# Kernel tuning notes

Hardware: AMD Instinct MI355X
Metric: run time of the kernel (lower is better)

## Reference

```python
import jax, jax.numpy as jnp
import numpy as np

NUM_CLASSES = 4   # Level has 4 contiguous classes 0..3
VMAX = 64         # discretized vital-sign codes live in [0, VMAX)
HID = 64
OUT = 768
IN_VS = 28


def casual_weighted(vs, labels):
    """Vectorized equivalent of Encoder.CasualWeighted.

    For row i, col c: prob = (# rows j with labels[j]==labels[i] and
    vs[j,c]==vs[i,c]) / (# rows with labels==labels[i]).  Returns vs * prob.
    """
    N, F = vs.shape
    vs_int = vs.astype(jnp.int32)                       # values are integer codes
    lab = labels.astype(jnp.int32)
    keys = lab[:, None] * VMAX + vs_int                 # [N, F] joint (class, value) key
    cols = jnp.arange(F)[None, :]                       # [1, F]
    counts = jnp.zeros((NUM_CLASSES * VMAX, F), jnp.float32).at[keys, cols].add(1.0)
    class_size = jnp.zeros((NUM_CLASSES,), jnp.float32).at[lab].add(1.0)
    prob = counts[keys, cols] / class_size[lab][:, None]  # [N, F]
    return vs * prob


def feature_extractor(x, W_ih, W_hh, b_ih, b_hh, W_fc, b_fc):
    """nn.LSTM over a length-1 sequence (h0=c0=0) followed by Linear."""
    h0 = jnp.zeros((x.shape[0], HID), x.dtype)
    gates = x @ W_ih.T + h0 @ W_hh.T + b_ih + b_hh      # [N, 4H], torch gate order i,f,g,o
    i, f, g, o = jnp.split(gates, 4, axis=-1)
    c = jax.nn.sigmoid(i) * jnp.tanh(g)                 # f*c0 = 0
    h = jax.nn.sigmoid(o) * jnp.tanh(c)
    return h @ W_fc.T + b_fc                            # [N, OUT]


def setup_inputs() -> dict:
    key = jax.random.key(0)
    ks = jax.random.split(key, 10)
    N = 100000
    VS = jax.random.randint(ks[0], (N, IN_VS), 0, VMAX).astype(jnp.float32)
    CC = jax.random.normal(ks[1], (N, 1, OUT), dtype=jnp.float32)
    Level = jax.random.randint(ks[2], (N,), 0, NUM_CLASSES).astype(jnp.int64)
    Depart = jax.random.randint(ks[3], (N,), 0, 10).astype(jnp.int64)
    s = 0.05
    W_ih = jax.random.normal(ks[4], (4 * HID, IN_VS), dtype=jnp.float32) * s
    W_hh = jax.random.normal(ks[5], (4 * HID, HID), dtype=jnp.float32) * s
    b_ih = jax.random.normal(ks[6], (4 * HID,), dtype=jnp.float32) * s
    b_hh = jax.random.normal(ks[7], (4 * HID,), dtype=jnp.float32) * s
    W_fc = jax.random.normal(ks[8], (OUT, HID), dtype=jnp.float32) * s
    b_fc = jax.random.normal(ks[9], (OUT,), dtype=jnp.float32) * s
    return {"VS": VS, "CC": CC, "Level": Level, "Depart": Depart,
            "W_ih": W_ih, "W_hh": W_hh, "b_ih": b_ih, "b_hh": b_hh,
            "W_fc": W_fc, "b_fc": b_fc}


def reference(VS, CC, Level, Depart, W_ih, W_hh, b_ih, b_hh, W_fc, b_fc):
    cc_feat = jnp.squeeze(CC)                           # [N, 768]
    vs_cw = casual_weighted(VS, Level)                  # [N, 28]
    vs_feat = feature_extractor(vs_cw, W_ih, W_hh, b_ih, b_hh, W_fc, b_fc)
    return (cc_feat, vs_feat, Level, Depart)
```

## Files before the change

kernel.cpp:

```cpp
#include <hip/hip_runtime.h>
#include <hip/hip_bf16.h>

#define N_ROWS 100000
#define F_VS 28
#define HIDN 64
#define OUT_F 768
#define NCLS 4
#define VMAXC 64

typedef __attribute__((ext_vector_type(8))) short short8;
typedef __attribute__((ext_vector_type(4))) float floatx4;


__device__ __forceinline__ float frcp(float x) { return __builtin_amdgcn_rcpf(x); }
__device__ __forceinline__ float sigm(float x) { return frcp(1.f + __expf(-x)); }
__device__ __forceinline__ float tanh_f(float x) { return 1.f - 2.f * frcp(__expf(2.f * x) + 1.f); }

__global__ __launch_bounds__(256) void k_hist(const float* __restrict__ VS,
                                              const int* __restrict__ Level,
                                              const float* __restrict__ Wfc,
                                              int* __restrict__ counts,
                                              int* __restrict__ cls,
                                              __hip_bfloat16* __restrict__ wfc16) {
    __shared__ int lc[NCLS * VMAXC * F_VS];
    __shared__ int lcls[NCLS];
    int tid = threadIdx.x;
    for (int i = tid; i < NCLS * VMAXC * F_VS; i += 256) lc[i] = 0;
    if (tid < NCLS) lcls[tid] = 0;

    int gtid = blockIdx.x * 256 + tid;
    int gsz = gridDim.x * 256;
    for (int i = gtid; i < OUT_F * HIDN; i += gsz)
        wfc16[i] = __float2bfloat16(Wfc[i]);
    __syncthreads();

    for (int i = gtid; i < N_ROWS; i += gsz) {
        int lab = Level[i];
        atomicAdd(&lcls[lab], 1);
        const float4* row = (const float4*)(VS + (size_t)i * F_VS);
#pragma unroll
        for (int q = 0; q < 7; q++) {
            float4 v4 = row[q];
            int c = q * 4;
            atomicAdd(&lc[((lab << 6) + (int)v4.x) * F_VS + c + 0], 1);
            atomicAdd(&lc[((lab << 6) + (int)v4.y) * F_VS + c + 1], 1);
            atomicAdd(&lc[((lab << 6) + (int)v4.z) * F_VS + c + 2], 1);
            atomicAdd(&lc[((lab << 6) + (int)v4.w) * F_VS + c + 3], 1);
        }
    }
    __syncthreads();
    for (int i = tid; i < NCLS * VMAXC * F_VS; i += 256) {
        int v = lc[i];
        if (v) atomicAdd(&counts[i], v);
    }
    if (tid < NCLS) {
        int v = lcls[tid];
        if (v) atomicAdd(&cls[tid], v);
    }
}

__global__ __launch_bounds__(256) void k_lstm(const float* __restrict__ VS,
                                              const int* __restrict__ Level,
                                              const int* __restrict__ Depart,
                                              const float* __restrict__ Wih,
                                              const float* __restrict__ bih,
                                              const float* __restrict__ bhh,
                                              const int* __restrict__ counts,
                                              const int* __restrict__ cls,
                                              __hip_bfloat16* __restrict__ h16,
                                              float* __restrict__ outL,
                                              float* __restrict__ outD) {
    int tid = threadIdx.x;
    int gtid = blockIdx.x * 256 + tid;

    if (gtid < N_ROWS) {
        outL[gtid] = (float)Level[gtid];
        outD[gtid] = (float)Depart[gtid];
    }

    int lane = tid & 63;
    int wib = tid >> 6;
    int w = gtid >> 6;
    int nw = (gridDim.x * 256) >> 6;

    float w0[F_VS], w2[F_VS], w3[F_VS];
#pragma unroll
    for (int j = 0; j < F_VS; j++) {
        w0[j] = Wih[(0 * HIDN + lane) * F_VS + j];
        w2[j] = Wih[(2 * HIDN + lane) * F_VS + j];
        w3[j] = Wih[(3 * HIDN + lane) * F_VS + j];
    }
    float b0 = bih[0 * HIDN + lane] + bhh[0 * HIDN + lane];
    float b2 = bih[2 * HIDN + lane] + bhh[2 * HIDN + lane];
    float b3 = bih[3 * HIDN + lane] + bhh[3 * HIDN + lane];

    __shared__ float xsh[4][64];

    for (int r = w; r < N_ROWS; r += nw) {
        int lab = Level[r];
        float inv = frcp((float)cls[lab]);
        float xv = 0.f;
        if (lane < F_VS) {
            float v = VS[(size_t)r * F_VS + lane];
            int vi = (int)v;
            int cnt = counts[(((lab << 6) | vi)) * F_VS + lane];
            xv = v * ((float)cnt * inv);
        }
        xsh[wib][lane] = xv;
        __asm__ volatile("" ::: "memory");

        float a0 = b0, a2 = b2, a3 = b3;
#pragma unroll
        for (int q = 0; q < 7; q++) {
            floatx4 xq = *(const floatx4*)(&xsh[wib][q * 4]);
            a0 = fmaf(xq[0], w0[4 * q + 0], a0);
            a0 = fmaf(xq[1], w0[4 * q + 1], a0);
            a0 = fmaf(xq[2], w0[4 * q + 2], a0);
            a0 = fmaf(xq[3], w0[4 * q + 3], a0);
            a2 = fmaf(xq[0], w2[4 * q + 0], a2);
            a2 = fmaf(xq[1], w2[4 * q + 1], a2);
            a2 = fmaf(xq[2], w2[4 * q + 2], a2);
            a2 = fmaf(xq[3], w2[4 * q + 3], a2);
            a3 = fmaf(xq[0], w3[4 * q + 0], a3);
            a3 = fmaf(xq[1], w3[4 * q + 1], a3);
            a3 = fmaf(xq[2], w3[4 * q + 2], a3);
            a3 = fmaf(xq[3], w3[4 * q + 3], a3);
        }
        __asm__ volatile("" ::: "memory");

        float c = sigm(a0) * tanh_f(a2);
        float h = sigm(a3) * tanh_f(c);
        h16[(size_t)r * HIDN + lane] = __float2bfloat16(h);
    }
}

__global__ __launch_bounds__(256) void k_gemm(const __hip_bfloat16* __restrict__ h16,
                                              const __hip_bfloat16* __restrict__ wfc16,
                                              const float* __restrict__ bfc,
                                              float* __restrict__ outV) {
    int tid = threadIdx.x;
    int lane = tid & 63;
    int w = (blockIdx.x * 256 + tid) >> 6;
    int nw = (gridDim.x * 256) >> 6;
    int quad = lane >> 4;
    int l16 = lane & 15;
    const int nm = N_ROWS / 16;

    for (int mt = w; mt < nm; mt += nw) {
        int row0 = mt * 16;
        const short* hA = (const short*)(h16 + (size_t)(row0 + l16) * HIDN + quad * 8);
        short8 a0 = *(const short8*)(hA);
        short8 a1 = *(const short8*)(hA + 32);
        for (int nt = 0; nt < OUT_F / 16; nt++) {
            const short* pB = (const short*)(wfc16 + (size_t)(nt * 16 + l16) * HIDN + quad * 8);
            short8 bf0 = *(const short8*)(pB);
            short8 bf1 = *(const short8*)(pB + 32);
            floatx4 acc = {0.f, 0.f, 0.f, 0.f};
            acc = __builtin_amdgcn_mfma_f32_16x16x32_bf16(a0, bf0, acc, 0, 0, 0);
            acc = __builtin_amdgcn_mfma_f32_16x16x32_bf16(a1, bf1, acc, 0, 0, 0);
            float bias = bfc[nt * 16 + l16];
#pragma unroll
            for (int rr = 0; rr < 4; rr++) {
                outV[(size_t)(row0 + quad * 4 + rr) * OUT_F + nt * 16 + l16] = acc[rr] + bias;
            }
        }
    }
}

__global__ __launch_bounds__(256) void k_copy(const float4* __restrict__ src,
                                              float4* __restrict__ dst, int n4) {
    int i = blockIdx.x * blockDim.x + threadIdx.x;
    int s = gridDim.x * blockDim.x;
    for (; i < n4; i += s) dst[i] = src[i];
}

extern "C" void kernel_launch(void* const* d_in, const int* in_sizes, int n_in,
                              void* d_out, int out_size, void* d_ws, size_t ws_size,
                              hipStream_t stream) {
    const float* VS = (const float*)d_in[0];
    const float* CC = (const float*)d_in[1];
    const int* Level = (const int*)d_in[2];
    const int* Depart = (const int*)d_in[3];
    const float* Wih = (const float*)d_in[4];
    const float* bih = (const float*)d_in[6];
    const float* bhh = (const float*)d_in[7];
    const float* Wfc = (const float*)d_in[8];
    const float* bfc = (const float*)d_in[9];

    float* out = (float*)d_out;
    char* ws = (char*)d_ws;
    int* counts = (int*)ws;
    int* cls = (int*)(ws + 28672);
    __hip_bfloat16* wfc16 = (__hip_bfloat16*)(ws + 28928);
    __hip_bfloat16* h16 = (__hip_bfloat16*)(ws + 131072);

    float* outCC = out;
    float* outV = out + (size_t)N_ROWS * OUT_F;
    float* outL = out + (size_t)2 * N_ROWS * OUT_F;
    float* outD = outL + N_ROWS;

    hipMemsetAsync(d_ws, 0, 28688, stream);
    k_hist<<<64, 256, 0, stream>>>(VS, Level, Wfc, counts, cls, wfc16);
    k_lstm<<<800, 256, 0, stream>>>(VS, Level, Depart, Wih, bih, bhh, counts, cls, h16, outL, outD);
    k_gemm<<<512, 256, 0, stream>>>(h16, wfc16, bfc, outV);
    k_copy<<<2048, 256, 0, stream>>>((const float4*)CC, (float4*)outCC,
                                     (N_ROWS * OUT_F) / 4);
}
```

Before: 925.3 us.

## Fuse LSTM, FC GEMM and CC copy into one kernel with block specialization

Merges the LSTM, the bf16 MFMA output GEMM and the CC/label copy into a single launch. Each wave computes 16 rows of hidden state into LDS and immediately runs the GEMM for that tile, so the h16 round trip through global memory disappears. A separate set of blocks handles the large CC copy and the label/depart outputs concurrently with the compute blocks. Launch overhead drops, but each wave now does a serial 16-row LSTM loop and the copy blocks compete for bandwidth with the outV stores.

```diff
diff --git a/kernel.cpp b/kernel.cpp
--- a/kernel.cpp
+++ b/kernel.cpp
@@ -7,6 +7,10 @@
 #define OUT_F 768
 #define NCLS 4
 #define VMAXC 64
+
+#define TILE_BLOCKS 1563
+#define COPY_BLOCKS 485
+#define GRID_FUSED (TILE_BLOCKS + COPY_BLOCKS)
 
 typedef __attribute__((ext_vector_type(8))) short short8;
 typedef __attribute__((ext_vector_type(4))) float floatx4;
@@ -59,29 +63,41 @@
     }
 }
 
-__global__ __launch_bounds__(256) void k_lstm(const float* __restrict__ VS,
-                                              const int* __restrict__ Level,
-                                              const int* __restrict__ Depart,
-                                              const float* __restrict__ Wih,
-                                              const float* __restrict__ bih,
-                                              const float* __restrict__ bhh,
-                                              const int* __restrict__ counts,
-                                              const int* __restrict__ cls,
-                                              __hip_bfloat16* __restrict__ h16,
-                                              float* __restrict__ outL,
-                                              float* __restrict__ outD) {
+__global__ __launch_bounds__(256) void k_fused(const float* __restrict__ VS,
+                                               const int* __restrict__ Level,
+                                               const int* __restrict__ Depart,
+                                               const float* __restrict__ Wih,
+                                               const float* __restrict__ bih,
+                                               const float* __restrict__ bhh,
+                                               const int* __restrict__ counts,
+                                               const int* __restrict__ cls,
+                                               const __hip_bfloat16* __restrict__ wfc16,
+                                               const float* __restrict__ bfc,
+                                               const float4* __restrict__ CC,
+                                               float4* __restrict__ outCC,
+                                               float* __restrict__ outV,
+                                               float* __restrict__ outL,
+                                               float* __restrict__ outD) {
     int tid = threadIdx.x;
-    int gtid = blockIdx.x * 256 + tid;
-
-    if (gtid < N_ROWS) {
-        outL[gtid] = (float)Level[gtid];
-        outD[gtid] = (float)Depart[gtid];
+
+    if (blockIdx.x >= TILE_BLOCKS) {
+        int cb = blockIdx.x - TILE_BLOCKS;
+        int ctid = cb * 256 + tid;
+        int csz = COPY_BLOCKS * 256;
+        for (int i = ctid; i < N_ROWS; i += csz) {
+            outL[i] = (float)Level[i];
+            outD[i] = (float)Depart[i];
+        }
+        const int n4 = (N_ROWS * OUT_F) / 4;
+        for (int i = ctid; i < n4; i += csz) outCC[i] = CC[i];
+        return;
     }
 
     int lane = tid & 63;
     int wib = tid >> 6;
-    int w = gtid >> 6;
-    int nw = (gridDim.x * 256) >> 6;
+    int wave = blockIdx.x * 4 + wib;
+    const int nm = N_ROWS / 16;
+    if (wave >= nm) return;
 
     float w0[F_VS], w2[F_VS], w3[F_VS];
 #pragma unroll
@@ -95,8 +111,12 @@
     float b3 = bih[3 * HIDN + lane] + bhh[3 * HIDN + lane];
 
     __shared__ float xsh[4][64];
-
-    for (int r = w; r < N_ROWS; r += nw) {
+    __shared__ short hsh[4][16][72];
+
+    int row0 = wave * 16;
+#pragma unroll 1
+    for (int i = 0; i < 16; i++) {
+        int r = row0 + i;
         int lab = Level[r];
         float inv = frcp((float)cls[lab]);
         float xv = 0.f;
@@ -130,48 +150,30 @@
 
         float c = sigm(a0) * tanh_f(a2);
         float h = sigm(a3) * tanh_f(c);
-        h16[(size_t)r * HIDN + lane] = __float2bfloat16(h);
-    }
-}
-
-__global__ __launch_bounds__(256) void k_gemm(const __hip_bfloat16* __restrict__ h16,
-                                              const __hip_bfloat16* __restrict__ wfc16,
-                                              const float* __restrict__ bfc,
-                                              float* __restrict__ outV) {
-    int tid = threadIdx.x;
-    int lane = tid & 63;
-    int w = (blockIdx.x * 256 + tid) >> 6;
-    int nw = (gridDim.x * 256) >> 6;
+        __hip_bfloat16 hb = __float2bfloat16(h);
+        hsh[wib][i][lane] = *(short*)&hb;
+    }
+    __asm__ volatile("" ::: "memory");
+
     int quad = lane >> 4;
     int l16 = lane & 15;
-    const int nm = N_ROWS / 16;
-
-    for (int mt = w; mt < nm; mt += nw) {
-        int row0 = mt * 16;
-        const short* hA = (const short*)(h16 + (size_t)(row0 + l16) * HIDN + quad * 8);
-        short8 a0 = *(const short8*)(hA);
-        short8 a1 = *(const short8*)(hA + 32);
-        for (int nt = 0; nt < OUT_F / 16; nt++) {
-            const short* pB = (const short*)(wfc16 + (size_t)(nt * 16 + l16) * HIDN + quad * 8);
-            short8 bf0 = *(const short8*)(pB);
-            short8 bf1 = *(const short8*)(pB + 32);
-            floatx4 acc = {0.f, 0.f, 0.f, 0.f};
-            acc = __builtin_amdgcn_mfma_f32_16x16x32_bf16(a0, bf0, acc, 0, 0, 0);
-            acc = __builtin_amdgcn_mfma_f32_16x16x32_bf16(a1, bf1, acc, 0, 0, 0);
-            float bias = bfc[nt * 16 + l16];
-#pragma unroll
-            for (int rr = 0; rr < 4; rr++) {
-                outV[(size_t)(row0 + quad * 4 + rr) * OUT_F + nt * 16 + l16] = acc[rr] + bias;
-            }
-        }
-    }
-}
-
-__global__ __launch_bounds__(256) void k_copy(const float4* __restrict__ src,
-                                              float4* __restrict__ dst, int n4) {
-    int i = blockIdx.x * blockDim.x + threadIdx.x;
-    int s = gridDim.x * blockDim.x;
-    for (; i < n4; i += s) dst[i] = src[i];
+    const short* hA = &hsh[wib][l16][quad * 8];
+    short8 a0v = *(const short8*)(hA);
+    short8 a1v = *(const short8*)(hA + 32);
+
+    for (int nt = 0; nt < OUT_F / 16; nt++) {
+        const short* pB = (const short*)(wfc16 + (size_t)(nt * 16 + l16) * HIDN + quad * 8);
+        short8 bf0 = *(const short8*)(pB);
+        short8 bf1 = *(const short8*)(pB + 32);
+        floatx4 acc = {0.f, 0.f, 0.f, 0.f};
+        acc = __builtin_amdgcn_mfma_f32_16x16x32_bf16(a0v, bf0, acc, 0, 0, 0);
+        acc = __builtin_amdgcn_mfma_f32_16x16x32_bf16(a1v, bf1, acc, 0, 0, 0);
+        float bias = bfc[nt * 16 + l16];
+#pragma unroll
+        for (int rr = 0; rr < 4; rr++) {
+            outV[(size_t)(row0 + quad * 4 + rr) * OUT_F + nt * 16 + l16] = acc[rr] + bias;
+        }
+    }
 }
 
 extern "C" void kernel_launch(void* const* d_in, const int* in_sizes, int n_in,
@@ -192,7 +194,6 @@
     int* counts = (int*)ws;
     int* cls = (int*)(ws + 28672);
     __hip_bfloat16* wfc16 = (__hip_bfloat16*)(ws + 28928);
-    __hip_bfloat16* h16 = (__hip_bfloat16*)(ws + 131072);
 
     float* outCC = out;
     float* outV = out + (size_t)N_ROWS * OUT_F;
@@ -201,8 +202,8 @@
 
     hipMemsetAsync(d_ws, 0, 28688, stream);
     k_hist<<<64, 256, 0, stream>>>(VS, Level, Wfc, counts, cls, wfc16);
-    k_lstm<<<800, 256, 0, stream>>>(VS, Level, Depart, Wih, bih, bhh, counts, cls, h16, outL, outD);
-    k_gemm<<<512, 256, 0, stream>>>(h16, wfc16, bfc, outV);
-    k_copy<<<2048, 256, 0, stream>>>((const float4*)CC, (float4*)outCC,
-                                     (N_ROWS * OUT_F) / 4);
+    k_fused<<<GRID_FUSED, 256, 0, stream>>>(VS, Level, Depart, Wih, bih, bhh,
+                                            counts, cls, wfc16, bfc,
+                                            (const float4*)CC, (float4*)outCC,
+                                            outV, outL, outD);
 }
```

After: 890.9 us. 3.7% less time.
